# Kernel tuning notes

Hardware: AMD Instinct MI355X
Metric: run time of the kernel (lower is better)

The kernel has to match this reference:

```python
import jax, jax.numpy as jnp
import numpy as np

S, B, D = 2048, 2, 1024   # seq_len, batch, d_model
H, Dh = 16, 64            # n_head, d_head (H*Dh == D)
LN_EPS = 1e-5


def _rel_shift(x):
    # x: [qlen, klen, bsz, n_head] -- standard Transformer-XL relative shift
    q, k, b, n = x.shape
    x = jnp.pad(x, ((0, 0), (1, 0), (0, 0), (0, 0)))  # [q, k+1, b, n]
    x = x.reshape(k + 1, q, b, n)[1:]                  # drop first row
    return x.reshape(q, k, b, n)


def setup_inputs() -> dict:
    key = jax.random.key(0)
    ks = jax.random.split(key, 8)
    s = 0.02
    return {
        "x":    jax.random.normal(ks[0], (S, B, D), jnp.float32),
        "r":    jax.random.normal(ks[1], (1, D), jnp.float32),          # learned pos vector
        "rw":   jax.random.normal(ks[2], (H, Dh), jnp.float32),          # content bias
        "rr":   jax.random.normal(ks[3], (H, Dh), jnp.float32),          # position bias
        "ln_g": jnp.ones((D,), jnp.float32),
        "ln_b": jnp.zeros((D,), jnp.float32),
        "Wqkv": jax.random.normal(ks[4], (D, 3 * H * Dh), jnp.float32) * s,
        "Wr":   jax.random.normal(ks[5], (D, H * Dh), jnp.float32) * s,
        "Wo":   jax.random.normal(ks[6], (H * Dh, D), jnp.float32) * s,
    }


def reference(x, r, rw, rr, ln_g, ln_b, Wqkv, Wr, Wo):
    # Pre-LayerNorm (dropout = identity in eval mode)
    mu = jnp.mean(x, axis=-1, keepdims=True)
    var = jnp.mean(jnp.square(x - mu), axis=-1, keepdims=True)
    xn = (x - mu) * jax.lax.rsqrt(var + LN_EPS) * ln_g + ln_b   # [S,B,D]

    # relative position input: r expanded over seq
    r_exp = jnp.broadcast_to(r, (S, D))                          # [S,D]

    qkv = xn @ Wqkv                                              # [S,B,3*H*Dh]
    q, k, v = jnp.split(qkv, 3, axis=-1)
    q = q.reshape(S, B, H, Dh)
    k = k.reshape(S, B, H, Dh)
    v = v.reshape(S, B, H, Dh)
    rk = (r_exp @ Wr).reshape(S, H, Dh)                          # [S,H,Dh]

    scale = 1.0 / np.sqrt(Dh).astype(np.float32)
    AC = jnp.einsum('ibnd,jbnd->ijbn', q + rw, k)                # content term
    BD = jnp.einsum('ibnd,jnd->ijbn', q + rr, rk)                # position term
    BD = _rel_shift(BD)
    attn = jax.nn.softmax((AC + BD) * scale, axis=1)             # over key axis j

    av = jnp.einsum('ijbn,jbnd->ibnd', attn, v).reshape(S, B, H * Dh)
    return xn + av @ Wo                                          # residual w/ normed input
```

## Files before the change

### kernel.cpp

```cpp
#include <hip/hip_runtime.h>

typedef unsigned short u16;
typedef __attribute__((ext_vector_type(8))) __bf16 bf16x8;
typedef __attribute__((ext_vector_type(8))) u16 u16x8;
typedef __attribute__((ext_vector_type(4))) float f32x4;
typedef __attribute__((ext_vector_type(16))) float f32x16;

__device__ __forceinline__ float bf2f(u16 u){
  union { unsigned int i; float f; } v; v.i = ((unsigned int)u) << 16; return v.f;
}
__device__ __forceinline__ u16 f2bf(float f){
  union { float f; unsigned int u; } v; v.f = f;
  unsigned int u = v.u;
  u += 0x7FFFu + ((u >> 16) & 1u);
  return (u16)(u >> 16);
}
__device__ __forceinline__ unsigned fbits(float f){
  union { float f; unsigned u; } v; v.f = f; return v.u;
}
__device__ __forceinline__ void gld_lds16(const u16* g, u16* l){
  __builtin_amdgcn_global_load_lds((const __attribute__((address_space(1))) unsigned int*)g,
                                   (__attribute__((address_space(3))) unsigned int*)l, 16, 0, 0);
}

__global__ __launch_bounds__(256) void transpose2_k(const float* __restrict__ Wqkv, u16* __restrict__ wqkvT,
                                                    const float* __restrict__ Wo, u16* __restrict__ woT,
                                                    float* __restrict__ rk0z){
  __shared__ float tile[32][33];
  const int tx = threadIdx.x, ty = threadIdx.y;
  const float* in; u16* out; int C, bxx;
  if(blockIdx.x < 96){ in = Wqkv; out = wqkvT; C = 3072; bxx = blockIdx.x; }
  else               { in = Wo;   out = woT;   C = 1024; bxx = blockIdx.x - 96; }
  const int R = 1024;
  if(blockIdx.x == 0 && blockIdx.y == 0){
    float4 z = {0.f, 0.f, 0.f, 0.f};
    reinterpret_cast<float4*>(rk0z)[ty * 32 + tx] = z;
  }
  const int bx = bxx * 32, by = blockIdx.y * 32;
  #pragma unroll
  for(int i = 0; i < 32; i += 8)
    tile[ty + i][tx] = in[(size_t)(by + ty + i) * C + bx + tx];
  __syncthreads();
  #pragma unroll
  for(int i = 0; i < 32; i += 8)
    out[(size_t)(bx + ty + i) * R + by + tx] = f2bf(tile[tx][ty + i]);
}

__global__ __launch_bounds__(256) void ln_k(const float* __restrict__ x, const float* __restrict__ gw,
                                            const float* __restrict__ bw, u16* __restrict__ xnb){
  const int row = blockIdx.x, t = threadIdx.x;
  const float* xr = x + (size_t)row * 1024;
  float4 xv = *reinterpret_cast<const float4*>(xr + t * 4);
  float s  = xv.x + xv.y + xv.z + xv.w;
  float s2 = xv.x*xv.x + xv.y*xv.y + xv.z*xv.z + xv.w*xv.w;
  #pragma unroll
  for(int m = 1; m <= 32; m <<= 1){ s += __shfl_xor(s, m, 64); s2 += __shfl_xor(s2, m, 64); }
  __shared__ float red[8];
  const int w = t >> 6, lane = t & 63;
  if(lane == 0){ red[w] = s; red[4 + w] = s2; }
  __syncthreads();
  float S1 = red[0] + red[1] + red[2] + red[3];
  float S2 = red[4] + red[5] + red[6] + red[7];
  float mu = S1 * (1.f/1024.f);
  float var = S2 * (1.f/1024.f) - mu * mu;
  float rstd = rsqrtf(var + 1e-5f);
  float4 gv = *reinterpret_cast<const float4*>(gw + t * 4);
  float4 bv = *reinterpret_cast<const float4*>(bw + t * 4);
  ushort4 o;
  o.x = f2bf((xv.x - mu) * rstd * gv.x + bv.x);
  o.y = f2bf((xv.y - mu) * rstd * gv.y + bv.y);
  o.z = f2bf((xv.z - mu) * rstd * gv.z + bv.z);
  o.w = f2bf((xv.w - mu) * rstd * gv.w + bv.w);
  *reinterpret_cast<ushort4*>(xnb + (size_t)row * 1024 + t * 4) = o;
}

__global__ __launch_bounds__(256) void rk0_k(const float* __restrict__ r, const float* __restrict__ Wr,
                                             float* __restrict__ rk0){
  const int n = blockIdx.x * 256 + threadIdx.x;
  const int d0 = blockIdx.y * 32;
  float acc = 0.f;
  for(int d = d0; d < d0 + 32; ++d)
    acc += r[d] * Wr[(size_t)d * 1024 + n];
  atomicAdd(&rk0[n], acc);
}

__global__ __launch_bounds__(256) void c_k(const u16* __restrict__ qk, const float* __restrict__ rr,
                                           const float* __restrict__ rk0, float* __restrict__ cc){
  const int w = threadIdx.x >> 6, lane = threadIdx.x & 63;
  const int ib = blockIdx.x * 4 + w;
  const u16* qp = qk + (size_t)ib * 2048 + lane * 16;
  u16x8 q0 = *reinterpret_cast<const u16x8*>(qp);
  u16x8 q1 = *reinterpret_cast<const u16x8*>(qp + 8);
  const float* rrp = rr + lane * 16;
  const float* rkp = rk0 + lane * 16;
  float s = 0.f;
  #pragma unroll
  for(int e = 0; e < 8; ++e){
    s += (bf2f(q0[e]) + rrp[e]) * rkp[e];
    s += (bf2f(q1[e]) + rrp[8 + e]) * rkp[8 + e];
  }
  s += __shfl_xor(s, 1, 64);
  s += __shfl_xor(s, 2, 64);
  if((lane & 3) == 0) cc[(size_t)ib * 16 + (lane >> 2)] = s;
}

__global__ __launch_bounds__(256) void vtrans_k(const u16* __restrict__ vnat, u16* __restrict__ vT){
  __shared__ u16 tl[128][40];
  const int t = threadIdx.x;
  const int i0 = blockIdx.x * 128, c0 = blockIdx.y * 32, b = blockIdx.z;
  {
    const int ii = t & 127, cs = (t >> 7) * 16;
    const u16* p = vnat + (size_t)((i0 + ii) * 2 + b) * 1024 + c0 + cs;
    *reinterpret_cast<u16x8*>(&tl[ii][cs])     = *reinterpret_cast<const u16x8*>(p);
    *reinterpret_cast<u16x8*>(&tl[ii][cs + 8]) = *reinterpret_cast<const u16x8*>(p + 8);
  }
  __syncthreads();
  const int dr = t & 31, seg = t >> 5;
  const int R = (b * 16 + (c0 >> 6)) * 64 + (c0 & 63) + dr;
  u16 tmp[16];
  #pragma unroll
  for(int e = 0; e < 16; ++e) tmp[e] = tl[seg * 16 + e][dr];
  u16* op = vT + (size_t)R * 2048 + i0 + seg * 16;
  *reinterpret_cast<u16x8*>(op)     = *reinterpret_cast<u16x8*>(&tmp[0]);
  *reinterpret_cast<u16x8*>(op + 8) = *reinterpret_cast<u16x8*>(&tmp[8]);
}

__global__ __launch_bounds__(256) void gemm_qkv_k(const u16* __restrict__ A, const u16* __restrict__ BT,
                                                  u16* __restrict__ Cb, u16* __restrict__ vnat){
  __shared__ u16 sA[2][128 * 32];
  __shared__ u16 sB[2][128 * 32];
  const int t = threadIdx.x;
  const int row0 = blockIdx.y * 128, col0 = blockIdx.x * 128;
  const int w = t >> 6, lane = t & 63, g = lane >> 4, lq = lane & 15;
  const int wr = (w >> 1) * 64, wc = (w & 1) * 64;
  const int K = 1024;
  f32x4 zero4 = {0.f, 0.f, 0.f, 0.f};
  f32x4 acc[4][4];
  #pragma unroll
  for(int mi = 0; mi < 4; ++mi)
    #pragma unroll
    for(int ni = 0; ni < 4; ++ni) acc[mi][ni] = zero4;

  for(int kt = 0; kt < K; kt += 64){
    #pragma unroll
    for(int ks = 0; ks < 2; ++ks){
      const int kk = kt + ks * 32;
      gld_lds16(A  + (size_t)(row0 +      (t >> 2)) * K + kk + (t & 3) * 8, &sA[ks][w * 512]);
      gld_lds16(A  + (size_t)(row0 + 64 + (t >> 2)) * K + kk + (t & 3) * 8, &sA[ks][2048 + w * 512]);
      gld_lds16(BT + (size_t)(col0 +      (t >> 2)) * K + kk + (t & 3) * 8, &sB[ks][w * 512]);
      gld_lds16(BT + (size_t)(col0 + 64 + (t >> 2)) * K + kk + (t & 3) * 8, &sB[ks][2048 + w * 512]);
    }
    __syncthreads();
    #pragma unroll
    for(int ks = 0; ks < 2; ++ks){
      bf16x8 af[4];
      #pragma unroll
      for(int mi = 0; mi < 4; ++mi)
        af[mi] = *reinterpret_cast<const bf16x8*>(&sA[ks][(wr + mi * 16 + lq) * 32 + g * 8]);
      #pragma unroll
      for(int ni = 0; ni < 4; ++ni){
        bf16x8 bfr = *reinterpret_cast<const bf16x8*>(&sB[ks][(wc + ni * 16 + lq) * 32 + g * 8]);
        #pragma unroll
        for(int mi = 0; mi < 4; ++mi)
          acc[mi][ni] = __builtin_amdgcn_mfma_f32_16x16x32_bf16(af[mi], bfr, acc[mi][ni], 0, 0, 0);
      }
    }
    __syncthreads();
  }
  if(blockIdx.x < 16){
    #pragma unroll
    for(int mi = 0; mi < 4; ++mi)
      #pragma unroll
      for(int ni = 0; ni < 4; ++ni)
        #pragma unroll
        for(int rg = 0; rg < 4; ++rg){
          const int row = row0 + wr + mi * 16 + g * 4 + rg;
          const int col = col0 + wc + ni * 16 + lq;
          Cb[(size_t)row * 2048 + col] = f2bf(acc[mi][ni][rg]);
        }
  } else {
    #pragma unroll
    for(int mi = 0; mi < 4; ++mi)
      #pragma unroll
      for(int ni = 0; ni < 4; ++ni)
        #pragma unroll
        for(int rg = 0; rg < 4; ++rg){
          const int row = row0 + wr + mi * 16 + g * 4 + rg;
          const int col = col0 + wc + ni * 16 + lq - 2048;
          vnat[(size_t)row * 1024 + col] = f2bf(acc[mi][ni][rg]);
        }
  }
}

__global__ __launch_bounds__(256) void gemm_out_k(const u16* __restrict__ A, const u16* __restrict__ BT,
                                                  const u16* __restrict__ res, float* __restrict__ Cf){
  __shared__ u16 sA[128 * 32];
  __shared__ u16 sB[64 * 32];
  const int t = threadIdx.x;
  const int row0 = blockIdx.y * 128, col0 = blockIdx.x * 64;
  const int w = t >> 6, lane = t & 63, g = lane >> 4, lq = lane & 15;
  const int wr = (w >> 1) * 64, wc = (w & 1) * 32;
  const int K = 1024, N = 1024;
  f32x4 zero4 = {0.f, 0.f, 0.f, 0.f};
  f32x4 acc[4][2];
  #pragma unroll
  for(int mi = 0; mi < 4; ++mi)
    #pragma unroll
    for(int ni = 0; ni < 2; ++ni) acc[mi][ni] = zero4;

  for(int kt = 0; kt < K; kt += 32){
    gld_lds16(A  + (size_t)(row0 +      (t >> 2)) * K + kt + (t & 3) * 8, &sA[w * 512]);
    gld_lds16(A  + (size_t)(row0 + 64 + (t >> 2)) * K + kt + (t & 3) * 8, &sA[2048 + w * 512]);
    gld_lds16(BT + (size_t)(col0 +      (t >> 2)) * K + kt + (t & 3) * 8, &sB[w * 512]);
    __syncthreads();
    bf16x8 af[4];
    #pragma unroll
    for(int mi = 0; mi < 4; ++mi)
      af[mi] = *reinterpret_cast<const bf16x8*>(&sA[(wr + mi * 16 + lq) * 32 + g * 8]);
    #pragma unroll
    for(int ni = 0; ni < 2; ++ni){
      bf16x8 bfr = *reinterpret_cast<const bf16x8*>(&sB[(wc + ni * 16 + lq) * 32 + g * 8]);
      #pragma unroll
      for(int mi = 0; mi < 4; ++mi)
        acc[mi][ni] = __builtin_amdgcn_mfma_f32_16x16x32_bf16(af[mi], bfr, acc[mi][ni], 0, 0, 0);
    }
    __syncthreads();
  }
  #pragma unroll
  for(int mi = 0; mi < 4; ++mi)
    #pragma unroll
    for(int ni = 0; ni < 2; ++ni)
      #pragma unroll
      for(int rg = 0; rg < 4; ++rg){
        const int row = row0 + wr + mi * 16 + g * 4 + rg;
        const int col = col0 + wc + ni * 16 + lq;
        Cf[(size_t)row * N + col] = acc[mi][ni][rg] + bf2f(res[(size_t)row * N + col]);
      }
}

__global__ __launch_bounds__(256) void attn_k(const u16* __restrict__ qk, const u16* __restrict__ vT,
                                              const float* __restrict__ rw, const float* __restrict__ cc,
                                              u16* __restrict__ av){
  constexpr int S = 2048, ST = 74;
  __shared__ u16 ks[2][64 * ST];
  __shared__ u16 vs[2][64 * ST];
  const int t = threadIdx.x;
  const int i0 = blockIdx.x * 128;
  const int bh = blockIdx.y;
  const int b = bh >> 4, h = bh & 15;
  const int w = t >> 6, lane = t & 63, m = lane & 31, q5 = lane >> 5;
  const int iw0 = i0 + w * 32;
  const int i_lane = iw0 + m;
  const float SC = 0.125f * 1.4426950408889634f;

  bf16x8 qf[4];
  {
    const u16* qp = qk + (size_t)(i_lane * 2 + b) * 2048 + h * 64;
    const float* rwp = rw + h * 64;
    #pragma unroll
    for(int kt = 0; kt < 4; ++kt){
      const int dbase = kt * 16 + q5 * 8;
      u16x8 qv = *reinterpret_cast<const u16x8*>(qp + dbase);
      u16x8 a;
      #pragma unroll
      for(int e = 0; e < 8; ++e) a[e] = f2bf((bf2f(qv[e]) + rwp[dbase + e]) * SC);
      qf[kt] = *reinterpret_cast<bf16x8*>(&a);
    }
  }
  const float ciL = cc[(size_t)(i_lane * 2 + b) * 16 + h] * SC;
  const float cpL = (i_lane + 1 < S) ? cc[(size_t)((i_lane + 1) * 2 + b) * 16 + h] * SC : 0.0f;

  f32x16 acc0, acc1, z16;
  #pragma unroll
  for(int e = 0; e < 16; ++e) z16[e] = 0.f;
  acc0 = z16; acc1 = z16;
  float rsum = 0.f;

  const int jr = t >> 2, c0 = (t & 3) * 16;
  {
    const u16* kp = qk + (size_t)(jr * 2 + b) * 2048 + 1024 + h * 64 + c0;
    *reinterpret_cast<u16x8*>(&ks[0][jr * ST + c0])     = *reinterpret_cast<const u16x8*>(kp);
    *reinterpret_cast<u16x8*>(&ks[0][jr * ST + c0 + 8]) = *reinterpret_cast<const u16x8*>(kp + 8);
    const u16* vp = vT + ((size_t)bh * 64 + jr) * 2048 + c0;
    *reinterpret_cast<u16x8*>(&vs[0][jr * ST + c0])     = *reinterpret_cast<const u16x8*>(vp);
    *reinterpret_cast<u16x8*>(&vs[0][jr * ST + c0 + 8]) = *reinterpret_cast<const u16x8*>(vp + 8);
  }
  __syncthreads();

  for(int n = 0; n < 32; ++n){
    const int p = n & 1;
    u16x8 k0, k1, v0, v1;
    const bool pre = (n + 1 < 32);
    if(pre){
      const int j0n = (n + 1) * 64;
      const u16* kp = qk + (size_t)((j0n + jr) * 2 + b) * 2048 + 1024 + h * 64 + c0;
      k0 = *reinterpret_cast<const u16x8*>(kp);
      k1 = *reinterpret_cast<const u16x8*>(kp + 8);
      const u16* vp = vT + ((size_t)bh * 64 + jr) * 2048 + j0n + c0;
      v0 = *reinterpret_cast<const u16x8*>(vp);
      v1 = *reinterpret_cast<const u16x8*>(vp + 8);
    }
    const int j0 = n * 64;
    bf16x8 pfrag[4];
    #pragma unroll
    for(int jt = 0; jt < 2; ++jt){
      const int tj0 = j0 + jt * 32;
      f32x16 s = z16;
      #pragma unroll
      for(int kt = 0; kt < 4; ++kt){
        bf16x8 ka = *reinterpret_cast<const bf16x8*>(&ks[p][(jt * 32 + m) * ST + kt * 16 + q5 * 8]);
        s = __builtin_amdgcn_mfma_f32_32x32x16_bf16(ka, qf[kt], s, 0, 0, 0);
      }
      float pv[16];
      if(tj0 + 31 <= iw0){
        #pragma unroll
        for(int r = 0; r < 16; ++r) pv[r] = __builtin_amdgcn_exp2f(s[r] + ciL);
      } else if(tj0 >= iw0 + 33){
        #pragma unroll
        for(int r = 0; r < 16; ++r) pv[r] = __builtin_amdgcn_exp2f(s[r] + cpL);
      } else {
        #pragma unroll
        for(int r = 0; r < 16; ++r){
          const int j = tj0 + (r & 3) + 8 * (r >> 2) + 4 * q5;
          const float t1 = (j <= i_lane) ? ciL : cpL;
          const float bdL = (j == i_lane + 1) ? 0.0f : t1;
          pv[r] = __builtin_amdgcn_exp2f(s[r] + bdL);
        }
      }
      #pragma unroll
      for(int r = 0; r < 16; ++r) rsum += pv[r];
      unsigned pk[8];
      #pragma unroll
      for(int q = 0; q < 8; ++q)
        pk[q] = __builtin_amdgcn_perm(fbits(pv[2 * q + 1]), fbits(pv[2 * q]), 0x07060302);
      unsigned sAx = (q5 == 0) ? pk[2] : pk[0];
      unsigned sAy = (q5 == 0) ? pk[3] : pk[1];
      unsigned rAx = (unsigned)__shfl_xor((int)sAx, 32, 64);
      unsigned rAy = (unsigned)__shfl_xor((int)sAy, 32, 64);
      unsigned sBx = (q5 == 0) ? pk[6] : pk[4];
      unsigned sBy = (q5 == 0) ? pk[7] : pk[5];
      unsigned rBx = (unsigned)__shfl_xor((int)sBx, 32, 64);
      unsigned rBy = (unsigned)__shfl_xor((int)sBy, 32, 64);
      union { unsigned u[4]; bf16x8 bf; } f0, f1;
      if(q5 == 0){
        f0.u[0] = pk[0]; f0.u[1] = pk[1]; f0.u[2] = rAx; f0.u[3] = rAy;
        f1.u[0] = pk[4]; f1.u[1] = pk[5]; f1.u[2] = rBx; f1.u[3] = rBy;
      } else {
        f0.u[0] = rAx; f0.u[1] = rAy; f0.u[2] = pk[2]; f0.u[3] = pk[3];
        f1.u[0] = rBx; f1.u[1] = rBy; f1.u[2] = pk[6]; f1.u[3] = pk[7];
      }
      pfrag[jt * 2 + 0] = f0.bf;
      pfrag[jt * 2 + 1] = f1.bf;
    }
    #pragma unroll
    for(int kt = 0; kt < 4; ++kt){
      bf16x8 va0 = *reinterpret_cast<const bf16x8*>(&vs[p][(m) * ST + kt * 16 + q5 * 8]);
      acc0 = __builtin_amdgcn_mfma_f32_32x32x16_bf16(va0, pfrag[kt], acc0, 0, 0, 0);
      bf16x8 va1 = *reinterpret_cast<const bf16x8*>(&vs[p][(32 + m) * ST + kt * 16 + q5 * 8]);
      acc1 = __builtin_amdgcn_mfma_f32_32x32x16_bf16(va1, pfrag[kt], acc1, 0, 0, 0);
    }
    if(pre){
      const int q2 = p ^ 1;
      *reinterpret_cast<u16x8*>(&ks[q2][jr * ST + c0])     = k0;
      *reinterpret_cast<u16x8*>(&ks[q2][jr * ST + c0 + 8]) = k1;
      *reinterpret_cast<u16x8*>(&vs[q2][jr * ST + c0])     = v0;
      *reinterpret_cast<u16x8*>(&vs[q2][jr * ST + c0 + 8]) = v1;
    }
    __syncthreads();
  }
  rsum += __shfl_xor(rsum, 32, 64);
  const float rinv = 1.0f / rsum;
  u16* op = av + (size_t)(i_lane * 2 + b) * 1024 + h * 64;
  #pragma unroll
  for(int dt = 0; dt < 2; ++dt){
    const f32x16& A = dt ? acc1 : acc0;
    #pragma unroll
    for(int rq = 0; rq < 4; ++rq){
      ushort4 o;
      o.x = f2bf(A[rq * 4 + 0] * rinv);
      o.y = f2bf(A[rq * 4 + 1] * rinv);
      o.z = f2bf(A[rq * 4 + 2] * rinv);
      o.w = f2bf(A[rq * 4 + 3] * rinv);
      const int d0 = dt * 32 + 8 * rq + 4 * q5;
      *reinterpret_cast<ushort4*>(op + d0) = o;
    }
  }
}

extern "C" void kernel_launch(void* const* d_in, const int* in_sizes, int n_in,
                              void* d_out, int out_size, void* d_ws, size_t ws_size,
                              hipStream_t stream){
  (void)in_sizes; (void)n_in; (void)out_size; (void)ws_size;
  const float* x    = (const float*)d_in[0];
  const float* r    = (const float*)d_in[1];
  const float* rw   = (const float*)d_in[2];
  const float* rr   = (const float*)d_in[3];
  const float* ln_g = (const float*)d_in[4];
  const float* ln_b = (const float*)d_in[5];
  const float* Wqkv = (const float*)d_in[6];
  const float* Wr   = (const float*)d_in[7];
  const float* Wo   = (const float*)d_in[8];
  char* ws = (char*)d_ws;
  u16*   xnb   = (u16*)(ws + 0);
  u16*   qk    = (u16*)(ws + 8388608);
  u16*   av    = (u16*)(ws + 25165824);
  u16*   woT   = (u16*)(ws + 33554432);
  u16*   wqkvT = (u16*)(ws + 35651584);
  u16*   vT    = (u16*)(ws + 41943040);
  float* rk0   = (float*)(ws + 50331648);
  float* cc    = (float*)(ws + 50335744);
  u16*   vnat  = av;
  float* out   = (float*)d_out;

  transpose2_k<<<dim3(128, 32), dim3(32, 8), 0, stream>>>(Wqkv, wqkvT, Wo, woT, rk0);
  ln_k<<<4096, 256, 0, stream>>>(x, ln_g, ln_b, xnb);
  rk0_k<<<dim3(4, 32), 256, 0, stream>>>(r, Wr, rk0);
  gemm_qkv_k<<<dim3(24, 32), 256, 0, stream>>>(xnb, wqkvT, qk, vnat);
  vtrans_k<<<dim3(16, 32, 2), 256, 0, stream>>>(vnat, vT);
  c_k<<<1024, 256, 0, stream>>>(qk, rr, rk0, cc);
  attn_k<<<dim3(16, 32), 256, 0, stream>>>(qk, vT, rw, cc, av);
  gemm_out_k<<<dim3(16, 32), 256, 0, stream>>>(av, woT, xnb, out);
}
```

Before: 231.1 us.

## Split attention over key range and fuse LayerNorm into weight-transpose prep kernel

The attention kernel splits the key dimension in two halves along a new grid z axis, doubling block count from 512 to 1024 to better fill the GPU. Each half writes unnormalized bf16 partial outputs and row sums, and a new combine kernel adds them and normalizes. It relies on no running max, so plain sums of exp are combinable. Separately, LayerNorm is merged into the transpose launch to save a kernel launch. The split adds an extra pass over the output and bf16 rounding of partial sums.

Measured after the change: 238.4 us. 3.1% more time.

```diff
diff --git a/kernel.cpp b/kernel.cpp
--- a/kernel.cpp
+++ b/kernel.cpp
@@ -23,15 +23,44 @@
                                    (__attribute__((address_space(3))) unsigned int*)l, 16, 0, 0);
 }
 
-__global__ __launch_bounds__(256) void transpose2_k(const float* __restrict__ Wqkv, u16* __restrict__ wqkvT,
-                                                    const float* __restrict__ Wo, u16* __restrict__ woT,
-                                                    float* __restrict__ rk0z){
+__global__ __launch_bounds__(256) void prep_k(const float* __restrict__ Wqkv, u16* __restrict__ wqkvT,
+                                              const float* __restrict__ Wo, u16* __restrict__ woT,
+                                              float* __restrict__ rk0z,
+                                              const float* __restrict__ x, const float* __restrict__ gw,
+                                              const float* __restrict__ bw, u16* __restrict__ xnb){
   __shared__ float tile[32][33];
+  __shared__ float red[8];
   const int tx = threadIdx.x, ty = threadIdx.y;
+  if(blockIdx.x >= 128){
+    const int row = (blockIdx.x - 128) * 32 + blockIdx.y;
+    const int t = ty * 32 + tx;
+    const float* xr = x + (size_t)row * 1024;
+    float4 xv = *reinterpret_cast<const float4*>(xr + t * 4);
+    float s  = xv.x + xv.y + xv.z + xv.w;
+    float s2 = xv.x*xv.x + xv.y*xv.y + xv.z*xv.z + xv.w*xv.w;
+    #pragma unroll
+    for(int m = 1; m <= 32; m <<= 1){ s += __shfl_xor(s, m, 64); s2 += __shfl_xor(s2, m, 64); }
+    const int w = t >> 6, lane = t & 63;
+    if(lane == 0){ red[w] = s; red[4 + w] = s2; }
+    __syncthreads();
+    float S1 = red[0] + red[1] + red[2] + red[3];
+    float S2 = red[4] + red[5] + red[6] + red[7];
+    float mu = S1 * (1.f/1024.f);
+    float var = S2 * (1.f/1024.f) - mu * mu;
+    float rstd = rsqrtf(var + 1e-5f);
+    float4 gv = *reinterpret_cast<const float4*>(gw + t * 4);
+    float4 bv = *reinterpret_cast<const float4*>(bw + t * 4);
+    ushort4 o;
+    o.x = f2bf((xv.x - mu) * rstd * gv.x + bv.x);
+    o.y = f2bf((xv.y - mu) * rstd * gv.y + bv.y);
+    o.z = f2bf((xv.z - mu) * rstd * gv.z + bv.z);
+    o.w = f2bf((xv.w - mu) * rstd * gv.w + bv.w);
+    *reinterpret_cast<ushort4*>(xnb + (size_t)row * 1024 + t * 4) = o;
+    return;
+  }
   const float* in; u16* out; int C, bxx;
   if(blockIdx.x < 96){ in = Wqkv; out = wqkvT; C = 3072; bxx = blockIdx.x; }
   else               { in = Wo;   out = woT;   C = 1024; bxx = blockIdx.x - 96; }
-  const int R = 1024;
   if(blockIdx.x == 0 && blockIdx.y == 0){
     float4 z = {0.f, 0.f, 0.f, 0.f};
     reinterpret_cast<float4*>(rk0z)[ty * 32 + tx] = z;
@@ -43,35 +72,7 @@
   __syncthreads();
   #pragma unroll
   for(int i = 0; i < 32; i += 8)
-    out[(size_t)(bx + ty + i) * R + by + tx] = f2bf(tile[tx][ty + i]);
-}
-
-__global__ __launch_bounds__(256) void ln_k(const float* __restrict__ x, const float* __restrict__ gw,
-                                            const float* __restrict__ bw, u16* __restrict__ xnb){
-  const int row = blockIdx.x, t = threadIdx.x;
-  const float* xr = x + (size_t)row * 1024;
-  float4 xv = *reinterpret_cast<const float4*>(xr + t * 4);
-  float s  = xv.x + xv.y + xv.z + xv.w;
-  float s2 = xv.x*xv.x + xv.y*xv.y + xv.z*xv.z + xv.w*xv.w;
-  #pragma unroll
-  for(int m = 1; m <= 32; m <<= 1){ s += __shfl_xor(s, m, 64); s2 += __shfl_xor(s2, m, 64); }
-  __shared__ float red[8];
-  const int w = t >> 6, lane = t & 63;
-  if(lane == 0){ red[w] = s; red[4 + w] = s2; }
-  __syncthreads();
-  float S1 = red[0] + red[1] + red[2] + red[3];
-  float S2 = red[4] + red[5] + red[6] + red[7];
-  float mu = S1 * (1.f/1024.f);
-  float var = S2 * (1.f/1024.f) - mu * mu;
-  float rstd = rsqrtf(var + 1e-5f);
-  float4 gv = *reinterpret_cast<const float4*>(gw + t * 4);
-  float4 bv = *reinterpret_cast<const float4*>(bw + t * 4);
-  ushort4 o;
-  o.x = f2bf((xv.x - mu) * rstd * gv.x + bv.x);
-  o.y = f2bf((xv.y - mu) * rstd * gv.y + bv.y);
-  o.z = f2bf((xv.z - mu) * rstd * gv.z + bv.z);
-  o.w = f2bf((xv.w - mu) * rstd * gv.w + bv.w);
-  *reinterpret_cast<ushort4*>(xnb + (size_t)row * 1024 + t * 4) = o;
+    out[(size_t)(bx + ty + i) * 1024 + by + tx] = f2bf(tile[tx][ty + i]);
 }
 
 __global__ __launch_bounds__(256) void rk0_k(const float* __restrict__ r, const float* __restrict__ Wr,
@@ -238,9 +239,10 @@
       }
 }
 
-__global__ __launch_bounds__(256) void attn_k(const u16* __restrict__ qk, const u16* __restrict__ vT,
-                                              const float* __restrict__ rw, const float* __restrict__ cc,
-                                              u16* __restrict__ av){
+template<int NITER, int SPLIT>
+__device__ __forceinline__ void attn_body(const u16* __restrict__ qk, const u16* __restrict__ vT,
+                                          const float* __restrict__ rw, const float* __restrict__ cc,
+                                          u16* __restrict__ outO, float* __restrict__ prs){
   constexpr int S = 2048, ST = 74;
   __shared__ u16 ks[2][64 * ST];
   __shared__ u16 vs[2][64 * ST];
@@ -248,6 +250,8 @@
   const int i0 = blockIdx.x * 128;
   const int bh = blockIdx.y;
   const int b = bh >> 4, h = bh & 15;
+  const int z = SPLIT ? blockIdx.z : 0;
+  const int jbase = z * (NITER * 64);
   const int w = t >> 6, lane = t & 63, m = lane & 31, q5 = lane >> 5;
   const int iw0 = i0 + w * 32;
   const int i_lane = iw0 + m;
@@ -278,21 +282,21 @@
 
   const int jr = t >> 2, c0 = (t & 3) * 16;
   {
-    const u16* kp = qk + (size_t)(jr * 2 + b) * 2048 + 1024 + h * 64 + c0;
+    const u16* kp = qk + (size_t)((jbase + jr) * 2 + b) * 2048 + 1024 + h * 64 + c0;
     *reinterpret_cast<u16x8*>(&ks[0][jr * ST + c0])     = *reinterpret_cast<const u16x8*>(kp);
     *reinterpret_cast<u16x8*>(&ks[0][jr * ST + c0 + 8]) = *reinterpret_cast<const u16x8*>(kp + 8);
-    const u16* vp = vT + ((size_t)bh * 64 + jr) * 2048 + c0;
+    const u16* vp = vT + ((size_t)bh * 64 + jr) * 2048 + jbase + c0;
     *reinterpret_cast<u16x8*>(&vs[0][jr * ST + c0])     = *reinterpret_cast<const u16x8*>(vp);
     *reinterpret_cast<u16x8*>(&vs[0][jr * ST + c0 + 8]) = *reinterpret_cast<const u16x8*>(vp + 8);
   }
   __syncthreads();
 
-  for(int n = 0; n < 32; ++n){
+  for(int n = 0; n < NITER; ++n){
     const int p = n & 1;
     u16x8 k0, k1, v0, v1;
-    const bool pre = (n + 1 < 32);
+    const bool pre = (n + 1 < NITER);
     if(pre){
-      const int j0n = (n + 1) * 64;
+      const int j0n = jbase + (n + 1) * 64;
       const u16* kp = qk + (size_t)((j0n + jr) * 2 + b) * 2048 + 1024 + h * 64 + c0;
       k0 = *reinterpret_cast<const u16x8*>(kp);
       k1 = *reinterpret_cast<const u16x8*>(kp + 8);
@@ -300,7 +304,7 @@
       v0 = *reinterpret_cast<const u16x8*>(vp);
       v1 = *reinterpret_cast<const u16x8*>(vp + 8);
     }
-    const int j0 = n * 64;
+    const int j0 = jbase + n * 64;
     bf16x8 pfrag[4];
     #pragma unroll
     for(int jt = 0; jt < 2; ++jt){
@@ -369,8 +373,13 @@
     __syncthreads();
   }
   rsum += __shfl_xor(rsum, 32, 64);
-  const float rinv = 1.0f / rsum;
-  u16* op = av + (size_t)(i_lane * 2 + b) * 1024 + h * 64;
+  float rinv = 1.0f;
+  if(SPLIT){
+    if(q5 == 0) prs[(size_t)z * 65536 + (size_t)(i_lane * 2 + b) * 16 + h] = rsum;
+  } else {
+    rinv = 1.0f / rsum;
+  }
+  u16* op = outO + (size_t)(i_lane * 2 + b) * 1024 + h * 64;
   #pragma unroll
   for(int dt = 0; dt < 2; ++dt){
     const f32x16& A = dt ? acc1 : acc0;
@@ -387,10 +396,39 @@
   }
 }
 
+__global__ __launch_bounds__(256) void attn_split_k(const u16* __restrict__ qk, const u16* __restrict__ vT,
+                                                    const float* __restrict__ rw, const float* __restrict__ cc,
+                                                    u16* __restrict__ po0, u16* __restrict__ po1,
+                                                    float* __restrict__ prs){
+  attn_body<16, 1>(qk, vT, rw, cc, (blockIdx.z == 0) ? po0 : po1, prs);
+}
+__global__ __launch_bounds__(256) void attn_full_k(const u16* __restrict__ qk, const u16* __restrict__ vT,
+                                                   const float* __restrict__ rw, const float* __restrict__ cc,
+                                                   u16* __restrict__ av){
+  attn_body<32, 0>(qk, vT, rw, cc, av, nullptr);
+}
+
+__global__ __launch_bounds__(256) void combine_k(const u16* __restrict__ po0, const u16* __restrict__ po1,
+                                                 const float* __restrict__ prs, u16* __restrict__ av){
+  const int row = blockIdx.x, t = threadIdx.x;
+  const int col = t * 4, h = t >> 4;
+  const float r0 = prs[(size_t)row * 16 + h];
+  const float r1 = prs[65536 + (size_t)row * 16 + h];
+  const float rinv = 1.0f / (r0 + r1);
+  ushort4 a = *reinterpret_cast<const ushort4*>(po0 + (size_t)row * 1024 + col);
+  ushort4 c = *reinterpret_cast<const ushort4*>(po1 + (size_t)row * 1024 + col);
+  ushort4 o;
+  o.x = f2bf((bf2f(a.x) + bf2f(c.x)) * rinv);
+  o.y = f2bf((bf2f(a.y) + bf2f(c.y)) * rinv);
+  o.z = f2bf((bf2f(a.z) + bf2f(c.z)) * rinv);
+  o.w = f2bf((bf2f(a.w) + bf2f(c.w)) * rinv);
+  *reinterpret_cast<ushort4*>(av + (size_t)row * 1024 + col) = o;
+}
+
 extern "C" void kernel_launch(void* const* d_in, const int* in_sizes, int n_in,
                               void* d_out, int out_size, void* d_ws, size_t ws_size,
                               hipStream_t stream){
-  (void)in_sizes; (void)n_in; (void)out_size; (void)ws_size;
+  (void)in_sizes; (void)n_in; (void)out_size;
   const float* x    = (const float*)d_in[0];
   const float* r    = (const float*)d_in[1];
   const float* rw   = (const float*)d_in[2];
@@ -409,15 +447,22 @@
   u16*   vT    = (u16*)(ws + 41943040);
   float* rk0   = (float*)(ws + 50331648);
   float* cc    = (float*)(ws + 50335744);
+  float* prs   = (float*)(ws + 50597888);
+  u16*   po0   = (u16*)(ws + 51122176);
   u16*   vnat  = av;
   float* out   = (float*)d_out;
-
-  transpose2_k<<<dim3(128, 32), dim3(32, 8), 0, stream>>>(Wqkv, wqkvT, Wo, woT, rk0);
-  ln_k<<<4096, 256, 0, stream>>>(x, ln_g, ln_b, xnb);
+  const bool split = (ws_size >= 59510784ull);
+
+  prep_k<<<dim3(256, 32), dim3(32, 8), 0, stream>>>(Wqkv, wqkvT, Wo, woT, rk0, x, ln_g, ln_b, xnb);
   rk0_k<<<dim3(4, 32), 256, 0, stream>>>(r, Wr, rk0);
   gemm_qkv_k<<<dim3(24, 32), 256, 0, stream>>>(xnb, wqkvT, qk, vnat);
   vtrans_k<<<dim3(16, 32, 2), 256, 0, stream>>>(vnat, vT);
   c_k<<<1024, 256, 0, stream>>>(qk, rr, rk0, cc);
-  attn_k<<<dim3(16, 32), 256, 0, stream>>>(qk, vT, rw, cc, av);
+  if(split){
+    attn_split_k<<<dim3(16, 32, 2), 256, 0, stream>>>(qk, vT, rw, cc, po0, av, prs);
+    combine_k<<<4096, 256, 0, stream>>>(po0, av, prs, av);
+  } else {
+    attn_full_k<<<dim3(16, 32), 256, 0, stream>>>(qk, vT, rw, cc, av);
+  }
   gemm_out_k<<<dim3(16, 32), 256, 0, stream>>>(av, woT, xnb, out);
 }
```

## Fuse prep kernels, V transpose into QKV GEMM, and c-term into attention

Applied to the files above, without the earlier changes.

Merges the weight transpose, rk0 projection and LayerNorm into one prep kernel (grid 257x32), removing the atomic accumulation and zero-init. The QKV GEMM now writes V directly in transposed layout through an LDS staging tile, which removes the separate vtrans kernel and the vnat round trip. The positional c-term dot products are computed inside the attention kernel from q rows i and i+1, so the c_k kernel and the cc buffer go away. This cuts eight launches to four and removes intermediate memory traffic, at the cost of more LDS use in the GEMM and an extra q-row load per attention lane.

Measured after the change: 226.1 us. 1.02x faster.

```diff
diff --git a/kernel.cpp b/kernel.cpp
--- a/kernel.cpp
+++ b/kernel.cpp
@@ -23,19 +23,62 @@
                                    (__attribute__((address_space(3))) unsigned int*)l, 16, 0, 0);
 }
 
-__global__ __launch_bounds__(256) void transpose2_k(const float* __restrict__ Wqkv, u16* __restrict__ wqkvT,
-                                                    const float* __restrict__ Wo, u16* __restrict__ woT,
-                                                    float* __restrict__ rk0z){
+__global__ __launch_bounds__(256) void prep_k(const float* __restrict__ Wqkv, u16* __restrict__ wqkvT,
+                                              const float* __restrict__ Wo, u16* __restrict__ woT,
+                                              const float* __restrict__ r, const float* __restrict__ Wr,
+                                              float* __restrict__ rk0,
+                                              const float* __restrict__ x, const float* __restrict__ gw,
+                                              const float* __restrict__ bw, u16* __restrict__ xnb){
   __shared__ float tile[32][33];
+  __shared__ float red[8];
   const int tx = threadIdx.x, ty = threadIdx.y;
+  const int t = ty * 32 + tx;
+  if(blockIdx.x == 128){
+    const int n = blockIdx.y * 32 + (t & 31);
+    const int chunk = t >> 5;
+    float acc = 0.f;
+    const int d0 = chunk * 128;
+    for(int d = d0; d < d0 + 128; ++d)
+      acc += r[d] * Wr[(size_t)d * 1024 + n];
+    tile[chunk][t & 31] = acc;
+    __syncthreads();
+    if(chunk == 0){
+      float s = 0.f;
+      #pragma unroll
+      for(int c = 0; c < 8; ++c) s += tile[c][t & 31];
+      rk0[n] = s;
+    }
+    return;
+  }
+  if(blockIdx.x >= 129){
+    const int row = (blockIdx.x - 129) * 32 + blockIdx.y;
+    const float* xr = x + (size_t)row * 1024;
+    float4 xv = *reinterpret_cast<const float4*>(xr + t * 4);
+    float s  = xv.x + xv.y + xv.z + xv.w;
+    float s2 = xv.x*xv.x + xv.y*xv.y + xv.z*xv.z + xv.w*xv.w;
+    #pragma unroll
+    for(int m = 1; m <= 32; m <<= 1){ s += __shfl_xor(s, m, 64); s2 += __shfl_xor(s2, m, 64); }
+    const int w = t >> 6, lane = t & 63;
+    if(lane == 0){ red[w] = s; red[4 + w] = s2; }
+    __syncthreads();
+    float S1 = red[0] + red[1] + red[2] + red[3];
+    float S2 = red[4] + red[5] + red[6] + red[7];
+    float mu = S1 * (1.f/1024.f);
+    float var = S2 * (1.f/1024.f) - mu * mu;
+    float rstd = rsqrtf(var + 1e-5f);
+    float4 gv = *reinterpret_cast<const float4*>(gw + t * 4);
+    float4 bv = *reinterpret_cast<const float4*>(bw + t * 4);
+    ushort4 o;
+    o.x = f2bf((xv.x - mu) * rstd * gv.x + bv.x);
+    o.y = f2bf((xv.y - mu) * rstd * gv.y + bv.y);
+    o.z = f2bf((xv.z - mu) * rstd * gv.z + bv.z);
+    o.w = f2bf((xv.w - mu) * rstd * gv.w + bv.w);
+    *reinterpret_cast<ushort4*>(xnb + (size_t)row * 1024 + t * 4) = o;
+    return;
+  }
   const float* in; u16* out; int C, bxx;
   if(blockIdx.x < 96){ in = Wqkv; out = wqkvT; C = 3072; bxx = blockIdx.x; }
   else               { in = Wo;   out = woT;   C = 1024; bxx = blockIdx.x - 96; }
-  const int R = 1024;
-  if(blockIdx.x == 0 && blockIdx.y == 0){
-    float4 z = {0.f, 0.f, 0.f, 0.f};
-    reinterpret_cast<float4*>(rk0z)[ty * 32 + tx] = z;
-  }
   const int bx = bxx * 32, by = blockIdx.y * 32;
   #pragma unroll
   for(int i = 0; i < 32; i += 8)
@@ -43,92 +86,14 @@
   __syncthreads();
   #pragma unroll
   for(int i = 0; i < 32; i += 8)
-    out[(size_t)(bx + ty + i) * R + by + tx] = f2bf(tile[tx][ty + i]);
-}
-
-__global__ __launch_bounds__(256) void ln_k(const float* __restrict__ x, const float* __restrict__ gw,
-                                            const float* __restrict__ bw, u16* __restrict__ xnb){
-  const int row = blockIdx.x, t = threadIdx.x;
-  const float* xr = x + (size_t)row * 1024;
-  float4 xv = *reinterpret_cast<const float4*>(xr + t * 4);
-  float s  = xv.x + xv.y + xv.z + xv.w;
-  float s2 = xv.x*xv.x + xv.y*xv.y + xv.z*xv.z + xv.w*xv.w;
-  #pragma unroll
-  for(int m = 1; m <= 32; m <<= 1){ s += __shfl_xor(s, m, 64); s2 += __shfl_xor(s2, m, 64); }
-  __shared__ float red[8];
-  const int w = t >> 6, lane = t & 63;
-  if(lane == 0){ red[w] = s; red[4 + w] = s2; }
-  __syncthreads();
-  float S1 = red[0] + red[1] + red[2] + red[3];
-  float S2 = red[4] + red[5] + red[6] + red[7];
-  float mu = S1 * (1.f/1024.f);
-  float var = S2 * (1.f/1024.f) - mu * mu;
-  float rstd = rsqrtf(var + 1e-5f);
-  float4 gv = *reinterpret_cast<const float4*>(gw + t * 4);
-  float4 bv = *reinterpret_cast<const float4*>(bw + t * 4);
-  ushort4 o;
-  o.x = f2bf((xv.x - mu) * rstd * gv.x + bv.x);
-  o.y = f2bf((xv.y - mu) * rstd * gv.y + bv.y);
-  o.z = f2bf((xv.z - mu) * rstd * gv.z + bv.z);
-  o.w = f2bf((xv.w - mu) * rstd * gv.w + bv.w);
-  *reinterpret_cast<ushort4*>(xnb + (size_t)row * 1024 + t * 4) = o;
-}
-
-__global__ __launch_bounds__(256) void rk0_k(const float* __restrict__ r, const float* __restrict__ Wr,
-                                             float* __restrict__ rk0){
-  const int n = blockIdx.x * 256 + threadIdx.x;
-  const int d0 = blockIdx.y * 32;
-  float acc = 0.f;
-  for(int d = d0; d < d0 + 32; ++d)
-    acc += r[d] * Wr[(size_t)d * 1024 + n];
-  atomicAdd(&rk0[n], acc);
-}
-
-__global__ __launch_bounds__(256) void c_k(const u16* __restrict__ qk, const float* __restrict__ rr,
-                                           const float* __restrict__ rk0, float* __restrict__ cc){
-  const int w = threadIdx.x >> 6, lane = threadIdx.x & 63;
-  const int ib = blockIdx.x * 4 + w;
-  const u16* qp = qk + (size_t)ib * 2048 + lane * 16;
-  u16x8 q0 = *reinterpret_cast<const u16x8*>(qp);
-  u16x8 q1 = *reinterpret_cast<const u16x8*>(qp + 8);
-  const float* rrp = rr + lane * 16;
-  const float* rkp = rk0 + lane * 16;
-  float s = 0.f;
-  #pragma unroll
-  for(int e = 0; e < 8; ++e){
-    s += (bf2f(q0[e]) + rrp[e]) * rkp[e];
-    s += (bf2f(q1[e]) + rrp[8 + e]) * rkp[8 + e];
-  }
-  s += __shfl_xor(s, 1, 64);
-  s += __shfl_xor(s, 2, 64);
-  if((lane & 3) == 0) cc[(size_t)ib * 16 + (lane >> 2)] = s;
-}
-
-__global__ __launch_bounds__(256) void vtrans_k(const u16* __restrict__ vnat, u16* __restrict__ vT){
-  __shared__ u16 tl[128][40];
-  const int t = threadIdx.x;
-  const int i0 = blockIdx.x * 128, c0 = blockIdx.y * 32, b = blockIdx.z;
-  {
-    const int ii = t & 127, cs = (t >> 7) * 16;
-    const u16* p = vnat + (size_t)((i0 + ii) * 2 + b) * 1024 + c0 + cs;
-    *reinterpret_cast<u16x8*>(&tl[ii][cs])     = *reinterpret_cast<const u16x8*>(p);
-    *reinterpret_cast<u16x8*>(&tl[ii][cs + 8]) = *reinterpret_cast<const u16x8*>(p + 8);
-  }
-  __syncthreads();
-  const int dr = t & 31, seg = t >> 5;
-  const int R = (b * 16 + (c0 >> 6)) * 64 + (c0 & 63) + dr;
-  u16 tmp[16];
-  #pragma unroll
-  for(int e = 0; e < 16; ++e) tmp[e] = tl[seg * 16 + e][dr];
-  u16* op = vT + (size_t)R * 2048 + i0 + seg * 16;
-  *reinterpret_cast<u16x8*>(op)     = *reinterpret_cast<u16x8*>(&tmp[0]);
-  *reinterpret_cast<u16x8*>(op + 8) = *reinterpret_cast<u16x8*>(&tmp[8]);
+    out[(size_t)(bx + ty + i) * 1024 + by + tx] = f2bf(tile[tx][ty + i]);
 }
 
 __global__ __launch_bounds__(256) void gemm_qkv_k(const u16* __restrict__ A, const u16* __restrict__ BT,
-                                                  u16* __restrict__ Cb, u16* __restrict__ vnat){
+                                                  u16* __restrict__ Cb, u16* __restrict__ vT){
   __shared__ u16 sA[2][128 * 32];
   __shared__ u16 sB[2][128 * 32];
+  __shared__ u16 tl[128 * 66];
   const int t = threadIdx.x;
   const int row0 = blockIdx.y * 128, col0 = blockIdx.x * 128;
   const int w = t >> 6, lane = t & 63, g = lane >> 4, lq = lane & 15;
@@ -179,16 +144,33 @@
           Cb[(size_t)row * 2048 + col] = f2bf(acc[mi][ni][rg]);
         }
   } else {
-    #pragma unroll
-    for(int mi = 0; mi < 4; ++mi)
-      #pragma unroll
-      for(int ni = 0; ni < 4; ++ni)
-        #pragma unroll
-        for(int rg = 0; rg < 4; ++rg){
-          const int row = row0 + wr + mi * 16 + g * 4 + rg;
-          const int col = col0 + wc + ni * 16 + lq - 2048;
-          vnat[(size_t)row * 1024 + col] = f2bf(acc[mi][ni][rg]);
-        }
+    const int cv0 = col0 - 2048;
+    #pragma unroll
+    for(int half = 0; half < 2; ++half){
+      if((w & 1) == half){
+        #pragma unroll
+        for(int mi = 0; mi < 4; ++mi)
+          #pragma unroll
+          for(int ni = 0; ni < 4; ++ni)
+            #pragma unroll
+            for(int rg = 0; rg < 4; ++rg)
+              tl[(wr + mi * 16 + g * 4 + rg) * 66 + ni * 16 + lq] = f2bf(acc[mi][ni][rg]);
+      }
+      __syncthreads();
+      const int h = (cv0 >> 6) + half;
+      const int b2 = w >> 1, dup = w & 1, d = lane;
+      const int R = (b2 * 16 + h) * 64 + d;
+      u16 tmp[32];
+      #pragma unroll
+      for(int e = 0; e < 32; ++e)
+        tmp[e] = tl[((dup * 32 + e) * 2 + b2) * 66 + d];
+      u16* op = vT + (size_t)R * 2048 + (row0 >> 1) + dup * 32;
+      *reinterpret_cast<u16x8*>(op)      = *reinterpret_cast<u16x8*>(&tmp[0]);
+      *reinterpret_cast<u16x8*>(op + 8)  = *reinterpret_cast<u16x8*>(&tmp[8]);
+      *reinterpret_cast<u16x8*>(op + 16) = *reinterpret_cast<u16x8*>(&tmp[16]);
+      *reinterpret_cast<u16x8*>(op + 24) = *reinterpret_cast<u16x8*>(&tmp[24]);
+      __syncthreads();
+    }
   }
 }
 
@@ -239,8 +221,8 @@
 }
 
 __global__ __launch_bounds__(256) void attn_k(const u16* __restrict__ qk, const u16* __restrict__ vT,
-                                              const float* __restrict__ rw, const float* __restrict__ cc,
-                                              u16* __restrict__ av){
+                                              const float* __restrict__ rw, const float* __restrict__ rr,
+                                              const float* __restrict__ rk0, u16* __restrict__ av){
   constexpr int S = 2048, ST = 74;
   __shared__ u16 ks[2][64 * ST];
   __shared__ u16 vs[2][64 * ST];
@@ -254,21 +236,37 @@
   const float SC = 0.125f * 1.4426950408889634f;
 
   bf16x8 qf[4];
+  float ciL, cpL;
   {
-    const u16* qp = qk + (size_t)(i_lane * 2 + b) * 2048 + h * 64;
-    const float* rwp = rw + h * 64;
+    const bool hasnext = (i_lane + 1 < S);
+    const u16* qp  = qk + (size_t)(i_lane * 2 + b) * 2048 + h * 64;
+    const u16* qp2 = qk + (size_t)((hasnext ? i_lane + 1 : i_lane) * 2 + b) * 2048 + h * 64;
+    const float* rwp = rw  + h * 64;
+    const float* rrp = rr  + h * 64;
+    const float* rkp = rk0 + h * 64;
+    float cpart = 0.f, cppart = 0.f;
     #pragma unroll
     for(int kt = 0; kt < 4; ++kt){
       const int dbase = kt * 16 + q5 * 8;
-      u16x8 qv = *reinterpret_cast<const u16x8*>(qp + dbase);
+      u16x8 qv  = *reinterpret_cast<const u16x8*>(qp  + dbase);
+      u16x8 qv2 = *reinterpret_cast<const u16x8*>(qp2 + dbase);
       u16x8 a;
       #pragma unroll
-      for(int e = 0; e < 8; ++e) a[e] = f2bf((bf2f(qv[e]) + rwp[dbase + e]) * SC);
+      for(int e = 0; e < 8; ++e){
+        const float qe  = bf2f(qv[e]);
+        const float rke = rkp[dbase + e];
+        const float rre = rrp[dbase + e];
+        a[e] = f2bf((qe + rwp[dbase + e]) * SC);
+        cpart  += (qe + rre) * rke;
+        cppart += (bf2f(qv2[e]) + rre) * rke;
+      }
       qf[kt] = *reinterpret_cast<bf16x8*>(&a);
     }
-  }
-  const float ciL = cc[(size_t)(i_lane * 2 + b) * 16 + h] * SC;
-  const float cpL = (i_lane + 1 < S) ? cc[(size_t)((i_lane + 1) * 2 + b) * 16 + h] * SC : 0.0f;
+    cpart  += __shfl_xor(cpart, 32, 64);
+    cppart += __shfl_xor(cppart, 32, 64);
+    ciL = cpart * SC;
+    cpL = hasnext ? cppart * SC : 0.0f;
+  }
 
   f32x16 acc0, acc1, z16;
   #pragma unroll
@@ -314,21 +312,21 @@
       float pv[16];
       if(tj0 + 31 <= iw0){
         #pragma unroll
-        for(int r = 0; r < 16; ++r) pv[r] = __builtin_amdgcn_exp2f(s[r] + ciL);
+        for(int r2 = 0; r2 < 16; ++r2) pv[r2] = __builtin_amdgcn_exp2f(s[r2] + ciL);
       } else if(tj0 >= iw0 + 33){
         #pragma unroll
-        for(int r = 0; r < 16; ++r) pv[r] = __builtin_amdgcn_exp2f(s[r] + cpL);
+        for(int r2 = 0; r2 < 16; ++r2) pv[r2] = __builtin_amdgcn_exp2f(s[r2] + cpL);
       } else {
         #pragma unroll
-        for(int r = 0; r < 16; ++r){
-          const int j = tj0 + (r & 3) + 8 * (r >> 2) + 4 * q5;
+        for(int r2 = 0; r2 < 16; ++r2){
+          const int j = tj0 + (r2 & 3) + 8 * (r2 >> 2) + 4 * q5;
           const float t1 = (j <= i_lane) ? ciL : cpL;
           const float bdL = (j == i_lane + 1) ? 0.0f : t1;
-          pv[r] = __builtin_amdgcn_exp2f(s[r] + bdL);
+          pv[r2] = __builtin_amdgcn_exp2f(s[r2] + bdL);
         }
       }
       #pragma unroll
-      for(int r = 0; r < 16; ++r) rsum += pv[r];
+      for(int r2 = 0; r2 < 16; ++r2) rsum += pv[r2];
       unsigned pk[8];
       #pragma unroll
       for(int q = 0; q < 8; ++q)
@@ -408,16 +406,11 @@
   u16*   wqkvT = (u16*)(ws + 35651584);
   u16*   vT    = (u16*)(ws + 41943040);
   float* rk0   = (float*)(ws + 50331648);
-  float* cc    = (float*)(ws + 50335744);
-  u16*   vnat  = av;
   float* out   = (float*)d_out;
 
-  transpose2_k<<<dim3(128, 32), dim3(32, 8), 0, stream>>>(Wqkv, wqkvT, Wo, woT, rk0);
-  ln_k<<<4096, 256, 0, stream>>>(x, ln_g, ln_b, xnb);
-  rk0_k<<<dim3(4, 32), 256, 0, stream>>>(r, Wr, rk0);
-  gemm_qkv_k<<<dim3(24, 32), 256, 0, stream>>>(xnb, wqkvT, qk, vnat);
-  vtrans_k<<<dim3(16, 32, 2), 256, 0, stream>>>(vnat, vT);
-  c_k<<<1024, 256, 0, stream>>>(qk, rr, rk0, cc);
-  attn_k<<<dim3(16, 32), 256, 0, stream>>>(qk, vT, rw, cc, av);
+  prep_k<<<dim3(257, 32), dim3(32, 8), 0, stream>>>(Wqkv, wqkvT, Wo, woT, r, Wr, rk0,
+                                                    x, ln_g, ln_b, xnb);
+  gemm_qkv_k<<<dim3(24, 32), 256, 0, stream>>>(xnb, wqkvT, qk, vT);
+  attn_k<<<dim3(16, 32), 256, 0, stream>>>(qk, vT, rw, rr, rk0, av);
   gemm_out_k<<<dim3(16, 32), 256, 0, stream>>>(av, woT, xnb, out);
 }
```
